# Performance work log

Hardware: AMD Instinct MI355X
Metric: run time of the kernel (lower is better)

Reference implementation:

```python
import jax, jax.numpy as jnp
import numpy as np

SPATIAL_SHAPES = np.array([[100, 100], [50, 50], [25, 25], [13, 13]], dtype=np.int32)
EMBED, NH, NL, NP = 256, 8, 4, 4
HD = EMBED // NH  # 32


def setup_inputs() -> dict:
    key = jax.random.key(0)
    ks = jax.random.split(key, 12)
    bs, nq = 4, 4000
    nv = int((SPATIAL_SHAPES[:, 0] * SPATIAL_SHAPES[:, 1]).sum())  # 13294
    s_lin = 1.0 / np.sqrt(EMBED)  # xavier-ish scale
    s_small = 0.02                # offsets/weights heads start near init
    return {
        "query": jax.random.normal(ks[0], (bs, nq, EMBED), jnp.float32),
        "value": jax.random.normal(ks[1], (bs, nv, EMBED), jnp.float32),
        "reference_points": jax.random.uniform(ks[2], (bs, nq, NL, 2), jnp.float32),
        "spatial_shapes": jnp.asarray(SPATIAL_SHAPES),
        "W_off": jax.random.normal(ks[3], (EMBED, NH * NL * NP * 2), jnp.float32) * s_small,
        "b_off": jax.random.normal(ks[4], (NH * NL * NP * 2,), jnp.float32) * s_small,
        "W_attn": jax.random.normal(ks[5], (EMBED, NH * NL * NP), jnp.float32) * s_small,
        "b_attn": jax.random.normal(ks[6], (NH * NL * NP,), jnp.float32) * s_small,
        "W_val": jax.random.normal(ks[7], (EMBED, EMBED), jnp.float32) * s_lin,
        "b_val": jnp.zeros((EMBED,), jnp.float32),
        "W_out": jax.random.normal(ks[8], (EMBED, EMBED), jnp.float32) * s_lin,
        "b_out": jnp.zeros((EMBED,), jnp.float32),
    }


def _bilinear_sample(val_l, H, W, x, y):
    """grid_sample(mode=bilinear, padding=zeros, align_corners=False) equivalent.
    val_l: [bs, nh, H*W, hd]; x, y: [bs, nh, nq, np] pixel-space coords.
    Returns [bs, nh, nq, np, hd]."""
    x0 = jnp.floor(x)
    y0 = jnp.floor(y)
    bs, nh, nq, npts = x.shape
    out = 0.0
    for dx, dy in ((0, 0), (1, 0), (0, 1), (1, 1)):
        xi = x0 + dx
        yi = y0 + dy
        w = (1.0 - jnp.abs(x - xi)) * (1.0 - jnp.abs(y - yi))
        valid = (xi >= 0) & (xi < W) & (yi >= 0) & (yi < H)
        idx = (jnp.clip(yi, 0, H - 1) * W + jnp.clip(xi, 0, W - 1)).astype(jnp.int32)
        g = jnp.take_along_axis(val_l, idx.reshape(bs, nh, nq * npts, 1), axis=2)
        g = g.reshape(bs, nh, nq, npts, -1)
        out = out + g * (w * valid.astype(w.dtype))[..., None]
    return out


def reference(query, value, reference_points, spatial_shapes,
              W_off, b_off, W_attn, b_attn, W_val, b_val, W_out, b_out):
    shapes = np.asarray(spatial_shapes)  # static level shapes
    bs, nq, _ = query.shape
    # value projection -> per-head layout [bs, nh, nv, hd]
    v = (value @ W_val + b_val).reshape(bs, -1, NH, HD).transpose(0, 2, 1, 3)
    # sampling offsets and attention weights from query
    off = (query @ W_off + b_off).reshape(bs, nq, NH, NL, NP, 2)
    attn = jax.nn.softmax((query @ W_attn + b_attn).reshape(bs, nq, NH, NL * NP), axis=-1)
    attn = attn.reshape(bs, nq, NH, NL, NP)
    # normalized sampling locations; normalizer = (W, H) per level
    normalizer = jnp.asarray(np.stack([shapes[:, 1], shapes[:, 0]], -1), jnp.float32)
    loc = reference_points[:, :, None, :, None, :] + off / normalizer[None, None, None, :, None, :]
    out = jnp.zeros((bs, NH, nq, HD), query.dtype)
    start = 0
    for l in range(NL):
        H, W = int(shapes[l, 0]), int(shapes[l, 1])
        val_l = v[:, :, start:start + H * W, :]
        # pixel coords with align_corners=False: p = loc*size - 0.5
        x = loc[:, :, :, l, :, 0].transpose(0, 2, 1, 3) * W - 0.5  # [bs,nh,nq,np]
        y = loc[:, :, :, l, :, 1].transpose(0, 2, 1, 3) * H - 0.5
        sampled = _bilinear_sample(val_l, H, W, x, y)  # [bs,nh,nq,np,hd]
        out = out + jnp.einsum('bhqpd,bqhp->bhqd', sampled, attn[:, :, :, l, :])
        start += H * W
    out = out.transpose(0, 2, 1, 3).reshape(bs, nq, EMBED)
    return out @ W_out + b_out
```

## Files before the change

kernel.cpp:

```cpp
#include <hip/hip_runtime.h>
#include <hip/hip_bf16.h>

#define EMBED 256
#define NH 8
#define NL 4
#define NP 4
#define HD 32
#define BS 4
#define NQ 4000
#define NV 13294

using f32x4   = __attribute__((ext_vector_type(4))) float;
using bf16x8  = __attribute__((ext_vector_type(8))) short;

__device__ __forceinline__ float bf2f_lo(unsigned u) {
    union { unsigned u; float f; } x; x.u = u << 16; return x.f;
}
__device__ __forceinline__ float bf2f_hi(unsigned u) {
    union { unsigned u; float f; } x; x.u = u & 0xffff0000u; return x.f;
}
__device__ __forceinline__ unsigned short f2bf(float f) {
    union { float f; unsigned u; } x; x.f = f;
    unsigned u = x.u;
    return (unsigned short)((u + 0x7fffu + ((u >> 16) & 1u)) >> 16);
}

__global__ void msda_prep_k(const float* __restrict__ W_val, const float* __restrict__ W_out,
                            const float* __restrict__ W_off, const float* __restrict__ W_attn,
                            const float* __restrict__ b_off, const float* __restrict__ b_attn,
                            unsigned short* __restrict__ Wt_val, unsigned short* __restrict__ Wt_out,
                            unsigned short* __restrict__ Wt_qa, float* __restrict__ b_qa) {
    int i = blockIdx.x * 256 + threadIdx.x;
    if (i < 384) b_qa[i] = (i < 256) ? b_off[i] : b_attn[i - 256];
    if (i < 65536) {
        int r = i >> 8, c = i & 255;
        Wt_val[c * 256 + r] = f2bf(W_val[i]);
    } else if (i < 131072) {
        int j = i - 65536, r = j >> 8, c = j & 255;
        Wt_out[c * 256 + r] = f2bf(W_out[j]);
    } else if (i < 229376) {
        int j = i - 131072;
        int n = j >> 8, k = j & 255;
        float v = (n < 256) ? W_off[k * 256 + n] : W_attn[k * 128 + (n - 256)];
        Wt_qa[j] = f2bf(v);
    }
}

template<int EPI, int AF32>
__global__ __launch_bounds__(256) void msda_gemm_k(
    const void* __restrict__ Ap,
    const unsigned short* __restrict__ Bt,
    const float* __restrict__ bias,
    void* __restrict__ out,
    int M, int N, int K)
{
    __shared__ __align__(16) unsigned short As[128][32];
    __shared__ __align__(16) unsigned short Bs[128][32];
    const int m0 = blockIdx.x * 128, n0 = blockIdx.y * 128;
    const int tid  = threadIdx.x;
    const int w    = tid >> 6;
    const int lane = tid & 63;
    const int quad = lane >> 4;
    const int l16  = lane & 15;
    const int wm   = w & 1, wn = w >> 1;
    const int sr   = tid >> 2;
    const int scol = (tid & 3) * 8;

    f32x4 acc[4][4];
#pragma unroll
    for (int a = 0; a < 4; a++)
#pragma unroll
        for (int b = 0; b < 4; b++) acc[a][b] = (f32x4){0.f, 0.f, 0.f, 0.f};

    const int ra0 = min(m0 + sr,      M - 1);
    const int ra1 = min(m0 + sr + 64, M - 1);
    const int rb0 = n0 + sr, rb1 = n0 + sr + 64;

    for (int k0 = 0; k0 < K; k0 += 32) {
        if (AF32) {
            const float* p = (const float*)Ap;
#pragma unroll
            for (int j = 0; j < 2; j++) {
                const float* src = p + (size_t)(j ? ra1 : ra0) * K + k0 + scol;
                float4 v0 = *(const float4*)(src);
                float4 v1 = *(const float4*)(src + 4);
                unsigned t[4];
                t[0] = f2bf(v0.x) | ((unsigned)f2bf(v0.y) << 16);
                t[1] = f2bf(v0.z) | ((unsigned)f2bf(v0.w) << 16);
                t[2] = f2bf(v1.x) | ((unsigned)f2bf(v1.y) << 16);
                t[3] = f2bf(v1.z) | ((unsigned)f2bf(v1.w) << 16);
                *(uint4*)&As[sr + j * 64][scol] = *(const uint4*)t;
            }
        } else {
            const unsigned short* p = (const unsigned short*)Ap;
            *(uint4*)&As[sr][scol]      = *(const uint4*)(p + (size_t)ra0 * K + k0 + scol);
            *(uint4*)&As[sr + 64][scol] = *(const uint4*)(p + (size_t)ra1 * K + k0 + scol);
        }
        *(uint4*)&Bs[sr][scol]      = *(const uint4*)(Bt + (size_t)rb0 * K + k0 + scol);
        *(uint4*)&Bs[sr + 64][scol] = *(const uint4*)(Bt + (size_t)rb1 * K + k0 + scol);
        __syncthreads();

        bf16x8 af[4], bfr[4];
#pragma unroll
        for (int mi = 0; mi < 4; mi++) af[mi]  = *(const bf16x8*)&As[wm * 64 + mi * 16 + l16][quad * 8];
#pragma unroll
        for (int ni = 0; ni < 4; ni++) bfr[ni] = *(const bf16x8*)&Bs[wn * 64 + ni * 16 + l16][quad * 8];
#pragma unroll
        for (int mi = 0; mi < 4; mi++)
#pragma unroll
            for (int ni = 0; ni < 4; ni++)
                acc[mi][ni] = __builtin_amdgcn_mfma_f32_16x16x32_bf16(af[mi], bfr[ni], acc[mi][ni], 0, 0, 0);
        __syncthreads();
    }

#pragma unroll
    for (int ni = 0; ni < 4; ni++) {
        int c = n0 + wn * 64 + ni * 16 + l16;
        float bvv = bias[c];
#pragma unroll
        for (int mi = 0; mi < 4; mi++) {
#pragma unroll
            for (int r = 0; r < 4; r++) {
                int m = m0 + wm * 64 + mi * 16 + quad * 4 + r;
                if (m >= M) continue;
                float val = acc[mi][ni][r] + bvv;
                if (EPI == 0) {
                    int b = m / NV, s = m % NV;
                    int h = c >> 5, d = c & 31;
                    ((unsigned short*)out)[(((size_t)(b * NH + h) * NV + s) << 5) + d] = f2bf(val);
                } else {
                    ((float*)out)[(size_t)m * N + c] = val;
                }
            }
        }
    }
}

__global__ __launch_bounds__(256) void msda_sampler_k(
    const float* __restrict__ refpts,
    const float* __restrict__ oa_buf,
    const unsigned short* __restrict__ v_buf,
    unsigned short* __restrict__ t_out)
{
    __shared__ float  oa_s[4][384];
    __shared__ float  ref_s[4][8];
    __shared__ float4 wtab[512];
    __shared__ int4   itab[512];

    const int tid = threadIdx.x;
    const int q0  = blockIdx.x * 4;

    {
        const float4* src = (const float4*)(oa_buf + (size_t)q0 * 384);
        float4* dst = (float4*)&oa_s[0][0];
        dst[tid] = src[tid];
        if (tid < 128) dst[256 + tid] = src[256 + tid];
        if (tid < 32) ((float*)ref_s)[tid] = refpts[q0 * 8 + tid];
    }
    __syncthreads();

    if (tid < 32) {
        float* lg = &oa_s[tid >> 3][256 + (tid & 7) * 16];
        float mx = -1e30f;
#pragma unroll
        for (int i = 0; i < 16; i++) mx = fmaxf(mx, lg[i]);
        float s = 0.f;
#pragma unroll
        for (int i = 0; i < 16; i++) { float e = __expf(lg[i] - mx); lg[i] = e; s += e; }
        float inv = 1.f / s;
#pragma unroll
        for (int i = 0; i < 16; i++) lg[i] *= inv;
    }
    __syncthreads();

    const int HWs[4]    = {100, 50, 25, 13};
    const int starts[4] = {0, 10000, 12500, 13125};
#pragma unroll
    for (int pt = tid; pt < 512; pt += 256) {
        int ql = pt >> 7, pid = pt & 127;
        int h = pid >> 4, l = (pid >> 2) & 3, p = pid & 3;
        int Wl = HWs[l];
        float fW = (float)Wl;
        float rx = ref_s[ql][l * 2], ry = ref_s[ql][l * 2 + 1];
        float offx = oa_s[ql][(h * 32) + l * 8 + p * 2];
        float offy = oa_s[ql][(h * 32) + l * 8 + p * 2 + 1];
        float a = oa_s[ql][256 + pid];
        float x = rx * fW + offx - 0.5f;
        float y = ry * fW + offy - 0.5f;
        float xf = floorf(x), yf = floorf(y);
        float fx = x - xf, fy = y - yf;
        int x0 = (int)xf, y0 = (int)yf;
        int x1 = x0 + 1, y1 = y0 + 1;
        float wx0 = (x0 >= 0 && x0 < Wl) ? (1.f - fx) : 0.f;
        float wx1 = (x1 >= 0 && x1 < Wl) ? fx : 0.f;
        float wy0 = (y0 >= 0 && y0 < Wl) ? (1.f - fy) : 0.f;
        float wy1 = (y1 >= 0 && y1 < Wl) ? fy : 0.f;
        int x0c = min(max(x0, 0), Wl - 1), x1c = min(max(x1, 0), Wl - 1);
        int y0c = min(max(y0, 0), Wl - 1), y1c = min(max(y1, 0), Wl - 1);
        int r0 = starts[l] + y0c * Wl, r1 = starts[l] + y1c * Wl;
        int ti = ((pid & 15) << 5) | (ql << 3) | h;
        wtab[ti] = make_float4(wx0 * wy0 * a, wx1 * wy0 * a, wx0 * wy1 * a, wx1 * wy1 * a);
        itab[ti] = make_int4(r0 + x0c, r0 + x1c, r1 + x0c, r1 + x1c);
    }
    __syncthreads();

    const int dg = tid & 7, h = (tid >> 3) & 7, ql = tid >> 6;
    const int q = q0 + ql;
    const int b = q / NQ;
    const unsigned short* vb = v_buf + ((size_t)(b * NH + h) * NV) * HD + dg * 4;
    const int tbase = (ql << 3) | h;

    float a0 = 0.f, a1 = 0.f, a2 = 0.f, a3 = 0.f;
#pragma unroll
    for (int lp = 0; lp < 16; lp++) {
        float4 wv = wtab[(lp << 5) | tbase];
        int4   ix = itab[(lp << 5) | tbase];
        uint2 s0 = *(const uint2*)(vb + (size_t)ix.x * HD);
        uint2 s1 = *(const uint2*)(vb + (size_t)ix.y * HD);
        uint2 s2 = *(const uint2*)(vb + (size_t)ix.z * HD);
        uint2 s3 = *(const uint2*)(vb + (size_t)ix.w * HD);
        a0 += wv.x * bf2f_lo(s0.x); a1 += wv.x * bf2f_hi(s0.x);
        a2 += wv.x * bf2f_lo(s0.y); a3 += wv.x * bf2f_hi(s0.y);
        a0 += wv.y * bf2f_lo(s1.x); a1 += wv.y * bf2f_hi(s1.x);
        a2 += wv.y * bf2f_lo(s1.y); a3 += wv.y * bf2f_hi(s1.y);
        a0 += wv.z * bf2f_lo(s2.x); a1 += wv.z * bf2f_hi(s2.x);
        a2 += wv.z * bf2f_lo(s2.y); a3 += wv.z * bf2f_hi(s2.y);
        a0 += wv.w * bf2f_lo(s3.x); a1 += wv.w * bf2f_hi(s3.x);
        a2 += wv.w * bf2f_lo(s3.y); a3 += wv.w * bf2f_hi(s3.y);
    }
    unsigned o0 = (unsigned)f2bf(a0) | ((unsigned)f2bf(a1) << 16);
    unsigned o1 = (unsigned)f2bf(a2) | ((unsigned)f2bf(a3) << 16);
    uint2 o = {o0, o1};
    *(uint2*)(t_out + (size_t)q * 256 + h * 32 + dg * 4) = o;
}

extern "C" void kernel_launch(void* const* d_in, const int* in_sizes, int n_in,
                              void* d_out, int out_size, void* d_ws, size_t ws_size,
                              hipStream_t stream) {
    const float* query  = (const float*)d_in[0];
    const float* value  = (const float*)d_in[1];
    const float* refpts = (const float*)d_in[2];
    const float* W_off  = (const float*)d_in[4];
    const float* b_off  = (const float*)d_in[5];
    const float* W_attn = (const float*)d_in[6];
    const float* b_attn = (const float*)d_in[7];
    const float* W_val  = (const float*)d_in[8];
    const float* b_val  = (const float*)d_in[9];
    const float* W_out  = (const float*)d_in[10];
    const float* b_out  = (const float*)d_in[11];

    char* wsp = (char*)d_ws;
    size_t o = 0;
    auto carve = [&](size_t bytes) -> void* {
        void* p = wsp + o; o += (bytes + 255) & ~(size_t)255; return p;
    };
    unsigned short* Wt_val = (unsigned short*)carve(256 * 256 * 2);
    unsigned short* Wt_out = (unsigned short*)carve(256 * 256 * 2);
    unsigned short* Wt_qa  = (unsigned short*)carve(384 * 256 * 2);
    float*          b_qa   = (float*)carve(384 * 4);
    unsigned short* v_buf  = (unsigned short*)carve((size_t)BS * NH * NV * HD * 2);
    float*          oa_buf = (float*)carve((size_t)BS * NQ * 384 * 4);
    unsigned short* t_buf  = (unsigned short*)carve((size_t)BS * NQ * 256 * 2);

    msda_prep_k<<<896, 256, 0, stream>>>(W_val, W_out, W_off, W_attn, b_off, b_attn,
                                         Wt_val, Wt_out, Wt_qa, b_qa);

    const int Mv = BS * NV;
    const int Mq = BS * NQ;
    msda_gemm_k<0, 1><<<dim3((Mv + 127) / 128, 2), 256, 0, stream>>>(value, Wt_val, b_val, v_buf, Mv, 256, 256);
    msda_gemm_k<1, 1><<<dim3(Mq / 128, 3), 256, 0, stream>>>(query, Wt_qa, b_qa, oa_buf, Mq, 384, 256);
    msda_sampler_k<<<Mq / 4, 256, 0, stream>>>(refpts, oa_buf, v_buf, t_buf);
    msda_gemm_k<1, 0><<<dim3(Mq / 128, 2), 256, 0, stream>>>(t_buf, Wt_out, b_out, (float*)d_out, Mq, 256, 256);
}
```

Baseline: 229.1 us.

## Pre-convert activations to bf16 and stream GEMM tiles via global_load_lds

Adds a standalone fp32-to-bf16 conversion kernel for value and query, so every GEMM now takes bf16 A operands. The GEMM tile loads become direct global-to-LDS async loads, each wave filling contiguous 1 KB segments. This removes per-tile conversion and register staging from the GEMM loop. The cost is an extra full pass of activation traffic and two more launches; workspace regions are aliased to keep the footprint small.

```diff
diff --git a/kernel.cpp b/kernel.cpp
--- a/kernel.cpp
+++ b/kernel.cpp
@@ -23,6 +23,24 @@
     union { float f; unsigned u; } x; x.f = f;
     unsigned u = x.u;
     return (unsigned short)((u + 0x7fffu + ((u >> 16) & 1u)) >> 16);
+}
+
+__device__ __forceinline__ void async16(const void* g, void* l) {
+    __builtin_amdgcn_global_load_lds(
+        (const __attribute__((address_space(1))) void*)g,
+        (__attribute__((address_space(3))) void*)l, 16, 0, 0);
+}
+
+__global__ __launch_bounds__(256) void msda_cvt_k(const float* __restrict__ in,
+                                                  unsigned short* __restrict__ out, int n4) {
+    int i = blockIdx.x * 256 + threadIdx.x;
+    if (i < n4) {
+        float4 v = ((const float4*)in)[i];
+        unsigned lo = f2bf(v.x) | ((unsigned)f2bf(v.y) << 16);
+        unsigned hi = f2bf(v.z) | ((unsigned)f2bf(v.w) << 16);
+        uint2 o = {lo, hi};
+        ((uint2*)out)[i] = o;
+    }
 }
 
 __global__ void msda_prep_k(const float* __restrict__ W_val, const float* __restrict__ W_out,
@@ -46,9 +64,9 @@
     }
 }
 
-template<int EPI, int AF32>
+template<int EPI>
 __global__ __launch_bounds__(256) void msda_gemm_k(
-    const void* __restrict__ Ap,
+    const unsigned short* __restrict__ A,
     const unsigned short* __restrict__ Bt,
     const float* __restrict__ bias,
     void* __restrict__ out,
@@ -63,8 +81,20 @@
     const int quad = lane >> 4;
     const int l16  = lane & 15;
     const int wm   = w & 1, wn = w >> 1;
-    const int sr   = tid >> 2;
-    const int scol = (tid & 3) * 8;
+
+    const int rseg = lane >> 2;
+    const int cb   = (lane & 3) * 16;
+    const int s0 = 2 * w, s1 = s0 + 1;
+    const int am0 = min(m0 + s0 * 16 + rseg, M - 1);
+    const int am1 = min(m0 + s1 * 16 + rseg, M - 1);
+    const char* agp0 = (const char*)(A  + (size_t)am0 * K) + cb;
+    const char* agp1 = (const char*)(A  + (size_t)am1 * K) + cb;
+    const char* bgp0 = (const char*)(Bt + (size_t)(n0 + s0 * 16 + rseg) * K) + cb;
+    const char* bgp1 = (const char*)(Bt + (size_t)(n0 + s1 * 16 + rseg) * K) + cb;
+    char* lA0 = (char*)&As[0][0] + s0 * 1024;
+    char* lA1 = (char*)&As[0][0] + s1 * 1024;
+    char* lB0 = (char*)&Bs[0][0] + s0 * 1024;
+    char* lB1 = (char*)&Bs[0][0] + s1 * 1024;
 
     f32x4 acc[4][4];
 #pragma unroll
@@ -72,32 +102,12 @@
 #pragma unroll
         for (int b = 0; b < 4; b++) acc[a][b] = (f32x4){0.f, 0.f, 0.f, 0.f};
 
-    const int ra0 = min(m0 + sr,      M - 1);
-    const int ra1 = min(m0 + sr + 64, M - 1);
-    const int rb0 = n0 + sr, rb1 = n0 + sr + 64;
-
     for (int k0 = 0; k0 < K; k0 += 32) {
-        if (AF32) {
-            const float* p = (const float*)Ap;
-#pragma unroll
-            for (int j = 0; j < 2; j++) {
-                const float* src = p + (size_t)(j ? ra1 : ra0) * K + k0 + scol;
-                float4 v0 = *(const float4*)(src);
-                float4 v1 = *(const float4*)(src + 4);
-                unsigned t[4];
-                t[0] = f2bf(v0.x) | ((unsigned)f2bf(v0.y) << 16);
-                t[1] = f2bf(v0.z) | ((unsigned)f2bf(v0.w) << 16);
-                t[2] = f2bf(v1.x) | ((unsigned)f2bf(v1.y) << 16);
-                t[3] = f2bf(v1.z) | ((unsigned)f2bf(v1.w) << 16);
-                *(uint4*)&As[sr + j * 64][scol] = *(const uint4*)t;
-            }
-        } else {
-            const unsigned short* p = (const unsigned short*)Ap;
-            *(uint4*)&As[sr][scol]      = *(const uint4*)(p + (size_t)ra0 * K + k0 + scol);
-            *(uint4*)&As[sr + 64][scol] = *(const uint4*)(p + (size_t)ra1 * K + k0 + scol);
-        }
-        *(uint4*)&Bs[sr][scol]      = *(const uint4*)(Bt + (size_t)rb0 * K + k0 + scol);
-        *(uint4*)&Bs[sr + 64][scol] = *(const uint4*)(Bt + (size_t)rb1 * K + k0 + scol);
+        const int kb = k0 * 2;
+        async16(agp0 + kb, lA0);
+        async16(agp1 + kb, lA1);
+        async16(bgp0 + kb, lB0);
+        async16(bgp1 + kb, lB1);
         __syncthreads();
 
         bf16x8 af[4], bfr[4];
@@ -259,16 +269,22 @@
     unsigned short* Wt_qa  = (unsigned short*)carve(384 * 256 * 2);
     float*          b_qa   = (float*)carve(384 * 4);
     unsigned short* v_buf  = (unsigned short*)carve((size_t)BS * NH * NV * HD * 2);
-    float*          oa_buf = (float*)carve((size_t)BS * NQ * 384 * 4);
-    unsigned short* t_buf  = (unsigned short*)carve((size_t)BS * NQ * 256 * 2);
+    char* regX = (char*)carve((size_t)BS * NV * EMBED * 2);
+    unsigned short* value_bf = (unsigned short*)regX;
+    float*          oa_buf   = (float*)regX;
+    char* regY = (char*)carve((size_t)BS * NQ * EMBED * 2);
+    unsigned short* query_bf = (unsigned short*)regY;
+    unsigned short* t_buf    = (unsigned short*)regY;
 
     msda_prep_k<<<896, 256, 0, stream>>>(W_val, W_out, W_off, W_attn, b_off, b_attn,
                                          Wt_val, Wt_out, Wt_qa, b_qa);
+    msda_cvt_k<<<(BS * NV * EMBED / 4 + 255) / 256, 256, 0, stream>>>(value, value_bf, BS * NV * EMBED / 4);
+    msda_cvt_k<<<(BS * NQ * EMBED / 4) / 256, 256, 0, stream>>>(query, query_bf, BS * NQ * EMBED / 4);
 
     const int Mv = BS * NV;
     const int Mq = BS * NQ;
-    msda_gemm_k<0, 1><<<dim3((Mv + 127) / 128, 2), 256, 0, stream>>>(value, Wt_val, b_val, v_buf, Mv, 256, 256);
-    msda_gemm_k<1, 1><<<dim3(Mq / 128, 3), 256, 0, stream>>>(query, Wt_qa, b_qa, oa_buf, Mq, 384, 256);
+    msda_gemm_k<0><<<dim3((Mv + 127) / 128, 2), 256, 0, stream>>>(value_bf, Wt_val, b_val, v_buf, Mv, 256, 256);
+    msda_gemm_k<1><<<dim3(Mq / 128, 3), 256, 0, stream>>>(query_bf, Wt_qa, b_qa, oa_buf, Mq, 384, 256);
     msda_sampler_k<<<Mq / 4, 256, 0, stream>>>(refpts, oa_buf, v_buf, t_buf);
-    msda_gemm_k<1, 0><<<dim3(Mq / 128, 2), 256, 0, stream>>>(t_buf, Wt_out, b_out, (float*)d_out, Mq, 256, 256);
-}
+    msda_gemm_k<1><<<dim3(Mq / 128, 2), 256, 0, stream>>>(t_buf, Wt_out, b_out, (float*)d_out, Mq, 256, 256);
+}
```

Result: slower. 236.7 us (+3.3%).
